# Kernel tuning notes

Measured on AMD Instinct MI355X. Metric: run time of the kernel, lower is better.

Reference implementation:

```python
import math
import jax, jax.numpy as jnp
import numpy as np

MODEL_DIM = 2048
NUM_HEADS = 16
HEAD_DIM = MODEL_DIM // NUM_HEADS
B, T = 4, 2048


def setup_inputs() -> dict:
    key = jax.random.key(0)
    ks = jax.random.split(key, 9)
    s = 0.02
    d = MODEL_DIM
    return {
        "x": jax.random.normal(ks[0], (B, T, d), dtype=jnp.float32),
        "wq": jax.random.normal(ks[1], (d, d), dtype=jnp.float32) * s,
        "bq": jnp.zeros((d,), dtype=jnp.float32),
        "wk": jax.random.normal(ks[2], (d, d), dtype=jnp.float32) * s,
        "bk": jnp.zeros((d,), dtype=jnp.float32),
        "wv": jax.random.normal(ks[3], (d, d), dtype=jnp.float32) * s,
        "bv": jnp.zeros((d,), dtype=jnp.float32),
        "wo": jax.random.normal(ks[4], (d, d), dtype=jnp.float32) * s,
        "bo": jnp.zeros((d,), dtype=jnp.float32),
    }


def reference(x, wq, bq, wk, bk, wv, bv, wo, bo):
    b, t, d = x.shape
    h, hd = NUM_HEADS, HEAD_DIM
    scale = 1.0 / math.sqrt(hd)
    # torch Linear: y = x @ W^T + b
    q = (x @ wq.T + bq).reshape(b, t, h, hd).transpose(0, 2, 1, 3)  # [B,H,T,hd]
    k = (x @ wk.T + bk).reshape(b, t, h, hd).transpose(0, 2, 1, 3)
    v = (x @ wv.T + bv).reshape(b, t, h, hd).transpose(0, 2, 1, 3)
    scores = jnp.einsum("bhqd,bhkd->bhqk", q, k) * scale  # [B,H,T,T]
    mask = jnp.tril(jnp.ones((t, t), dtype=bool))
    scores = jnp.where(mask[None, None], scores, -jnp.inf)
    probs = jax.nn.softmax(scores, axis=-1)
    out = jnp.einsum("bhqk,bhkd->bhqd", probs, v)  # [B,H,T,hd]
    out = out.transpose(0, 2, 1, 3).reshape(b, t, d)
    out = out @ wo.T + bo
    return (out, k, v)
```

## Files before the change

### kernel.cpp

```cpp
#include <hip/hip_runtime.h>
#include <hip/hip_bf16.h>
#include <stdint.h>

typedef __attribute__((ext_vector_type(8))) short short8;
typedef __attribute__((ext_vector_type(4))) float f32x4;

#define DEVI __device__ __forceinline__

DEVI unsigned short f2bf(float f) {
  union { float f; unsigned int u; } c; c.f = f;
  unsigned int u = c.u;
  u += 0x7fffu + ((u >> 16) & 1u);
  return (unsigned short)(u >> 16);
}

DEVI void gl_lds16(const void* gsrc, void* lds) {
  __builtin_amdgcn_global_load_lds(
      (const __attribute__((address_space(1))) unsigned int*)gsrc,
      (__attribute__((address_space(3))) unsigned int*)lds, 16, 0, 0);
}

#define MFMA(a, b, c) __builtin_amdgcn_mfma_f32_16x16x32_bf16((a), (b), (c), 0, 0, 0)

__global__ void cvt_f32_bf16(const float* __restrict__ in,
                             unsigned short* __restrict__ out, int n4) {
  const int stride = gridDim.x * blockDim.x;
  for (int i = blockIdx.x * blockDim.x + threadIdx.x; i < n4; i += stride) {
    const float4 v = ((const float4*)in)[i];
    ushort4 o;
    o.x = f2bf(v.x); o.y = f2bf(v.y); o.z = f2bf(v.z); o.w = f2bf(v.w);
    ((ushort4*)out)[i] = o;
  }
}


template<int MODE>
__global__ __launch_bounds__(512, 2)
void gemm256(const unsigned short* __restrict__ A,
             const unsigned short* __restrict__ Bw,
             const float* __restrict__ bq,
             const float* __restrict__ bk,
             const float* __restrict__ bv,
             float* __restrict__ Kf,
             float* __restrict__ Vf,
             unsigned short* __restrict__ Qpk,
             unsigned short* __restrict__ Kpk,
             unsigned short* __restrict__ Vpk,
             float* __restrict__ Cf,
             int M, int N, int K)
{
  __shared__ unsigned short S[4][16384];
  const int tid  = threadIdx.x;
  const int lane = tid & 63;
  const int wid  = tid >> 6;
  const int l15  = lane & 15, l4 = lane >> 4;

  const int chunk = gridDim.x >> 3;
  const int q  = blockIdx.x;
  const int wg = (q & 7) * chunk + (q >> 3);
  const int bm = (wg & 31) * 256;
  const int bn = (wg >> 5) * 256;

  const unsigned short* Asrc0 = A  + (size_t)(bm + wid * 16 + l15) * K + l4 * 8;
  const unsigned short* Asrc1 = A  + (size_t)(bm + (wid + 8) * 16 + l15) * K + l4 * 8;
  const unsigned short* Bsrc0 = Bw + (size_t)(bn + wid * 16 + l15) * K + l4 * 8;
  const unsigned short* Bsrc1 = Bw + (size_t)(bn + (wid + 8) * 16 + l15) * K + l4 * 8;

  const int nt = K >> 5;
#pragma unroll
  for (int kt = 0; kt < 3; ++kt) {
    unsigned short* Sd = S[kt];
    const int koff = kt * 32;
    gl_lds16(Asrc0 + koff, &Sd[wid * 512 + lane * 8]);
    gl_lds16(Asrc1 + koff, &Sd[(wid + 8) * 512 + lane * 8]);
    gl_lds16(Bsrc0 + koff, &Sd[8192 + wid * 512 + lane * 8]);
    gl_lds16(Bsrc1 + koff, &Sd[8192 + (wid + 8) * 512 + lane * 8]);
  }

  f32x4 acc[8][4] = {};
  const int afbase = (wid >> 2) * 4096 + lane * 8;
  const int bfbase = 8192 + (wid & 3) * 2048 + lane * 8;

  for (int kt = 0; kt < nt; ++kt) {
    const int rem = nt - 1 - kt;
    if (rem >= 2)      asm volatile("s_waitcnt vmcnt(8)" ::: "memory");
    else if (rem == 1) asm volatile("s_waitcnt vmcnt(4)" ::: "memory");
    else               asm volatile("s_waitcnt vmcnt(0)" ::: "memory");
    asm volatile("s_waitcnt lgkmcnt(0)" ::: "memory");
    __builtin_amdgcn_s_barrier();
    __builtin_amdgcn_sched_barrier(0);

    const unsigned short* Sb = S[kt & 3];
    short8 af[8], bf[4];
#pragma unroll
    for (int m = 0; m < 8; ++m) af[m] = *(const short8*)&Sb[afbase + m * 512];
#pragma unroll
    for (int n = 0; n < 4; ++n) bf[n] = *(const short8*)&Sb[bfbase + n * 512];

    if (kt + 3 < nt) {
      unsigned short* Sd = S[(kt + 3) & 3];
      const int koff = (kt + 3) * 32;
      gl_lds16(Asrc0 + koff, &Sd[wid * 512 + lane * 8]);
      gl_lds16(Asrc1 + koff, &Sd[(wid + 8) * 512 + lane * 8]);
      gl_lds16(Bsrc0 + koff, &Sd[8192 + wid * 512 + lane * 8]);
      gl_lds16(Bsrc1 + koff, &Sd[8192 + (wid + 8) * 512 + lane * 8]);
    }

    __builtin_amdgcn_s_setprio(1);
#pragma unroll
    for (int m = 0; m < 8; ++m)
#pragma unroll
      for (int n = 0; n < 4; ++n)
        acc[m][n] = MFMA(af[m], bf[n], acc[m][n]);
    __builtin_amdgcn_s_setprio(0);
  }

  const int rbase = l4 * 4;
#pragma unroll
  for (int m = 0; m < 8; ++m) {
    const int row0 = bm + (wid >> 2) * 128 + m * 16 + rbase;
#pragma unroll
    for (int n = 0; n < 4; ++n) {
      const int col6 = bn + (wid & 3) * 64 + n * 16 + l15;
      if constexpr (MODE == 3) {
        const float bb = bq[col6];
#pragma unroll
        for (int r = 0; r < 4; ++r)
          Cf[(size_t)(row0 + r) * N + col6] = acc[m][n][r] + bb;
      } else {
        const int sel = col6 >> 11;
        const int col = col6 & 2047;
        const float bb = (sel == 0 ? bq : sel == 1 ? bk : bv)[col];
        float vv[4];
#pragma unroll
        for (int r = 0; r < 4; ++r) vv[r] = acc[m][n][r] + bb;
        const int bI = row0 >> 11, t0 = row0 & 2047;
        const int h = col >> 7, e = col & 127;
        const size_t hb = ((size_t)(bI * 16 + h)) * 262144;
        if (sel == 0) {
          const size_t qb = hb + (size_t)(t0 >> 4) * 2048 + (e >> 5) * 512
                          + (t0 & 15) * 32 + (e & 31);
#pragma unroll
          for (int r = 0; r < 4; ++r) Qpk[qb + (size_t)r * 32] = f2bf(vv[r]);
        } else if (sel == 1) {
          const size_t idx = hb + (size_t)t0 * 128 + e;
          const size_t qb = hb + (size_t)(t0 >> 4) * 2048 + (e >> 5) * 512
                          + (t0 & 15) * 32 + (e & 31);
#pragma unroll
          for (int r = 0; r < 4; ++r) {
            Kf[idx + (size_t)r * 128] = vv[r];
            Kpk[qb + (size_t)r * 32] = f2bf(vv[r]);
          }
        } else {
          const size_t idx = hb + (size_t)t0 * 128 + e;
#pragma unroll
          for (int r = 0; r < 4; ++r) Vf[idx + (size_t)r * 128] = vv[r];
          const size_t vb = hb + (size_t)(t0 >> 6) * 8192 + (size_t)(e >> 4) * 1024
                          + ((t0 >> 5) & 1) * 512 + (e & 15) * 32 + (t0 & 31);
          ushort4 pk;
          pk.x = f2bf(vv[0]); pk.y = f2bf(vv[1]);
          pk.z = f2bf(vv[2]); pk.w = f2bf(vv[3]);
          *(ushort4*)&Vpk[vb] = pk;
        }
      }
    }
  }
}

__global__ __launch_bounds__(256, 2)
void attn_fwd(const unsigned short* __restrict__ Qf,
              const unsigned short* __restrict__ Kf,
              const unsigned short* __restrict__ Vf,
              unsigned short* __restrict__ Ab)
{
  constexpr float scale = 0.08838834764831843f;
  __shared__ unsigned short Pl[4][32][72];

  const int bid = blockIdx.x;
  const int idx = bid >> 3;
  const int bh  = (bid & 7) * 8 + (idx & 7);
  const int qb  = 15 - (idx >> 3);
  const int bI = bh >> 4, h = bh & 15;
  const int tid = threadIdx.x;
  const int wid = tid >> 6, lane = tid & 63;
  const int lr = lane & 15, lg = lane >> 4;
  const int lfo = lr * 32 + lg * 8;
  const int qw = qb * 128 + wid * 32;

  const unsigned short* Qp = Qf + (size_t)bh * 262144 + (size_t)(qw >> 4) * 2048;
  const unsigned short* Kp = Kf + (size_t)bh * 262144;
  const unsigned short* Vp = Vf + (size_t)bh * 262144;

  short8 qf[2][4];
#pragma unroll
  for (int m = 0; m < 2; ++m)
#pragma unroll
    for (int ks = 0; ks < 4; ++ks)
      qf[m][ks] = *(const short8*)&Qp[m * 2048 + ks * 512 + lfo];

  f32x4 o[2][8] = {};
  float mrun[2][4], lrun[2][4];
#pragma unroll
  for (int m = 0; m < 2; ++m)
#pragma unroll
    for (int r = 0; r < 4; ++r) { mrun[m][r] = -1e30f; lrun[m][r] = 0.f; }

  const int nfull = qw >> 6;
  for (int kt = 0; kt <= nfull; ++kt) {
    const int kv0 = kt * 64;
    const bool diag = (kt == nfull);
    const unsigned short* Kt = Kp + (size_t)(kv0 >> 4) * 2048;
    const unsigned short* Vt = Vp + (size_t)(kv0 >> 6) * 8192;

    short8 kf[4][4];
#pragma unroll
    for (int n = 0; n < 4; ++n)
#pragma unroll
      for (int ks = 0; ks < 4; ++ks)
        kf[n][ks] = *(const short8*)&Kt[n * 2048 + ks * 512 + lfo];
    f32x4 s[2][4] = {};
#pragma unroll
    for (int ks = 0; ks < 4; ++ks)
#pragma unroll
      for (int m = 0; m < 2; ++m)
#pragma unroll
        for (int n = 0; n < 4; ++n)
          s[m][n] = MFMA(qf[m][ks], kf[n][ks], s[m][n]);

    short8 vf[2][8];
#pragma unroll
    for (int ks2 = 0; ks2 < 2; ++ks2)
#pragma unroll
      for (int dt = 0; dt < 8; ++dt)
        vf[ks2][dt] = *(const short8*)&Vt[dt * 1024 + ks2 * 512 + lfo];

    float tmax[2][4];
#pragma unroll
    for (int m = 0; m < 2; ++m)
#pragma unroll
      for (int r = 0; r < 4; ++r) tmax[m][r] = -1e30f;
#pragma unroll
    for (int m = 0; m < 2; ++m)
#pragma unroll
      for (int n = 0; n < 4; ++n) {
        const int kg = kv0 + n * 16 + lr;
#pragma unroll
        for (int r = 0; r < 4; ++r) {
          float sv = s[m][n][r] * scale;
          if (diag) {
            const int qg = qw + m * 16 + lg * 4 + r;
            sv = (kg <= qg) ? sv : -1e30f;
          }
          s[m][n][r] = sv;
          tmax[m][r] = fmaxf(tmax[m][r], sv);
        }
      }
#pragma unroll
    for (int m = 0; m < 2; ++m)
#pragma unroll
      for (int r = 0; r < 4; ++r) {
#pragma unroll
        for (int off = 8; off >= 1; off >>= 1)
          tmax[m][r] = fmaxf(tmax[m][r], __shfl_xor(tmax[m][r], off));
        const float mnew  = fmaxf(mrun[m][r], tmax[m][r]);
        const float alpha = __expf(mrun[m][r] - mnew);
        mrun[m][r] = mnew;
        lrun[m][r] *= alpha;
#pragma unroll
        for (int d = 0; d < 8; ++d) o[m][d][r] *= alpha;
      }
#pragma unroll
    for (int m = 0; m < 2; ++m) {
      float ls[4] = {0.f, 0.f, 0.f, 0.f};
#pragma unroll
      for (int n = 0; n < 4; ++n)
#pragma unroll
        for (int r = 0; r < 4; ++r) {
          const float p = __expf(s[m][n][r] - mrun[m][r]);
          s[m][n][r] = p;
          ls[r] += p;
        }
#pragma unroll
      for (int r = 0; r < 4; ++r) {
#pragma unroll
        for (int off = 8; off >= 1; off >>= 1) ls[r] += __shfl_xor(ls[r], off);
        lrun[m][r] += ls[r];
      }
#pragma unroll
      for (int n = 0; n < 4; ++n)
#pragma unroll
        for (int r = 0; r < 4; ++r)
          Pl[wid][m * 16 + lg * 4 + r][n * 16 + lr] = f2bf(s[m][n][r]);
    }
#pragma unroll
    for (int ks2 = 0; ks2 < 2; ++ks2) {
      short8 pa[2];
#pragma unroll
      for (int m = 0; m < 2; ++m)
        pa[m] = *(const short8*)&Pl[wid][m * 16 + lr][ks2 * 32 + lg * 8];
#pragma unroll
      for (int dt = 0; dt < 8; ++dt)
#pragma unroll
        for (int m = 0; m < 2; ++m)
          o[m][dt] = MFMA(pa[m], vf[ks2][dt], o[m][dt]);
    }
  }
#pragma unroll
  for (int m = 0; m < 2; ++m)
#pragma unroll
    for (int r = 0; r < 4; ++r) {
      const float inv = 1.0f / lrun[m][r];
      const int t = qw + m * 16 + lg * 4 + r;
      unsigned short* dst = Ab + ((size_t)(bI * 2048 + t)) * 2048 + h * 128;
#pragma unroll
      for (int dt = 0; dt < 8; ++dt)
        dst[dt * 16 + lr] = f2bf(o[m][dt][r] * inv);
    }
}

extern "C" void kernel_launch(void* const* d_in, const int* in_sizes, int n_in,
                              void* d_out, int out_size, void* d_ws, size_t ws_size,
                              hipStream_t stream) {
  const float* x  = (const float*)d_in[0];
  const float* wq = (const float*)d_in[1];
  const float* bq = (const float*)d_in[2];
  const float* wk = (const float*)d_in[3];
  const float* bk = (const float*)d_in[4];
  const float* wv = (const float*)d_in[5];
  const float* bv = (const float*)d_in[6];
  const float* wo = (const float*)d_in[7];
  const float* bo = (const float*)d_in[8];

  float* out  = (float*)d_out;
  float* kout = out + (size_t)16777216;
  float* vout = out + (size_t)33554432;

  unsigned short* xb  = (unsigned short*)d_ws;
  unsigned short* wqb = xb  + 16777216;
  unsigned short* wkb = wqb + 4194304;
  unsigned short* wvb = wkb + 4194304;
  unsigned short* wob = wvb + 4194304;
  unsigned short* Qw  = wob + 4194304;
  unsigned short* Kw  = Qw  + 16777216;
  unsigned short* Vfw = Kw  + 16777216;
  unsigned short* Aw  = Vfw + 16777216;

  const int M = 8192, K = 2048;

  cvt_f32_bf16<<<1024, 256, 0, stream>>>(x,  xb,  4194304);
  cvt_f32_bf16<<<256,  256, 0, stream>>>(wq, wqb, 1048576);
  cvt_f32_bf16<<<256,  256, 0, stream>>>(wk, wkb, 1048576);
  cvt_f32_bf16<<<256,  256, 0, stream>>>(wv, wvb, 1048576);
  cvt_f32_bf16<<<256,  256, 0, stream>>>(wo, wob, 1048576);

  gemm256<0><<<dim3(768), 512, 0, stream>>>(xb, wqb, bq, bk, bv,
                                            kout, vout, Qw, Kw, Vfw,
                                            nullptr, M, 6144, K);

  attn_fwd<<<dim3(1024), 256, 0, stream>>>(Qw, Kw, Vfw, Aw);

  gemm256<3><<<dim3(256), 512, 0, stream>>>(Aw, wob, bo, nullptr, nullptr,
                                            nullptr, nullptr, nullptr, nullptr, nullptr,
                                            out, M, 2048, K);
}
```

Before: 575.1 us.

## Restructure GEMM into 8-phase ping-pong pipeline with 64-wide K tiles

```diff
diff --git a/kernel.cpp b/kernel.cpp
--- a/kernel.cpp
+++ b/kernel.cpp
@@ -21,6 +21,8 @@
 }
 
 #define MFMA(a, b, c) __builtin_amdgcn_mfma_f32_16x16x32_bf16((a), (b), (c), 0, 0, 0)
+#define BAR()  __builtin_amdgcn_s_barrier()
+#define SCHED0() __builtin_amdgcn_sched_barrier(0)
 
 __global__ void cvt_f32_bf16(const float* __restrict__ in,
                              unsigned short* __restrict__ out, int n4) {
@@ -36,24 +38,25 @@
 
 template<int MODE>
 __global__ __launch_bounds__(512, 2)
-void gemm256(const unsigned short* __restrict__ A,
-             const unsigned short* __restrict__ Bw,
-             const float* __restrict__ bq,
-             const float* __restrict__ bk,
-             const float* __restrict__ bv,
-             float* __restrict__ Kf,
-             float* __restrict__ Vf,
-             unsigned short* __restrict__ Qpk,
-             unsigned short* __restrict__ Kpk,
-             unsigned short* __restrict__ Vpk,
-             float* __restrict__ Cf,
-             int M, int N, int K)
+void gemm8p(const unsigned short* __restrict__ A,
+            const unsigned short* __restrict__ Bw,
+            const float* __restrict__ bq,
+            const float* __restrict__ bk,
+            const float* __restrict__ bv,
+            float* __restrict__ Kf,
+            float* __restrict__ Vf,
+            unsigned short* __restrict__ Qpk,
+            unsigned short* __restrict__ Kpk,
+            unsigned short* __restrict__ Vpk,
+            float* __restrict__ Cf,
+            int M, int N, int K)
 {
-  __shared__ unsigned short S[4][16384];
+  __shared__ unsigned short S[2][32768];
   const int tid  = threadIdx.x;
   const int lane = tid & 63;
   const int wid  = tid >> 6;
   const int l15  = lane & 15, l4 = lane >> 4;
+  const int wm   = wid >> 2, wn = wid & 3;
 
   const int chunk = gridDim.x >> 3;
   const int q  = blockIdx.x;
@@ -61,67 +64,123 @@
   const int bm = (wg & 31) * 256;
   const int bn = (wg >> 5) * 256;
 
-  const unsigned short* Asrc0 = A  + (size_t)(bm + wid * 16 + l15) * K + l4 * 8;
-  const unsigned short* Asrc1 = A  + (size_t)(bm + (wid + 8) * 16 + l15) * K + l4 * 8;
-  const unsigned short* Bsrc0 = Bw + (size_t)(bn + wid * 16 + l15) * K + l4 * 8;
-  const unsigned short* Bsrc1 = Bw + (size_t)(bn + (wid + 8) * 16 + l15) * K + l4 * 8;
-
-  const int nt = K >> 5;
-#pragma unroll
-  for (int kt = 0; kt < 3; ++kt) {
-    unsigned short* Sd = S[kt];
-    const int koff = kt * 32;
-    gl_lds16(Asrc0 + koff, &Sd[wid * 512 + lane * 8]);
-    gl_lds16(Asrc1 + koff, &Sd[(wid + 8) * 512 + lane * 8]);
-    gl_lds16(Bsrc0 + koff, &Sd[8192 + wid * 512 + lane * 8]);
-    gl_lds16(Bsrc1 + koff, &Sd[8192 + (wid + 8) * 512 + lane * 8]);
+  const unsigned short* Asrc = A  + (size_t)(bm + (wid >> 1) * 16 + l15) * K + (wid & 1) * 32 + l4 * 8;
+  const unsigned short* Bsrc = Bw + (size_t)(bn + (wid >> 1) * 16 + l15) * K + (wid & 1) * 32 + l4 * 8;
+
+  const int nKt   = K >> 6;
+  const int HTmax = nKt * 4;
+
+  auto stage_ht = [&](int g) {
+    if (g >= HTmax) return;
+    const int t = g >> 2, sub = g & 3, buf = t & 1, k0 = t << 6;
+#pragma unroll
+    for (int cc = 0; cc < 2; ++cc) {
+      if (sub >= 2) {
+        const int c = (sub - 2) * 2 + cc;
+        gl_lds16(Asrc + (size_t)(c * 64) * K + k0,
+                 &S[buf][c * 4096 + wid * 512 + lane * 8]);
+      } else {
+        const int c = sub * 2 + cc;
+        gl_lds16(Bsrc + (size_t)(c * 64) * K + k0,
+                 &S[buf][16384 + c * 4096 + wid * 512 + lane * 8]);
+      }
+    }
+  };
+
+#pragma unroll
+  for (int g = 0; g < 7; ++g) stage_ht(g);
+  asm volatile("s_waitcnt vmcnt(6)" ::: "memory");
+  SCHED0();
+  BAR();
+
+  f32x4 acc[8][4] = {};
+  short8 a[4][2], b[4][2];
+
+  for (int t = 0; t < nKt; ++t) {
+    const unsigned short* Sb = S[t & 1];
+    const int P = t * 4;
+
+#pragma unroll
+    for (int i = 0; i < 4; ++i)
+#pragma unroll
+      for (int ks = 0; ks < 2; ++ks)
+        a[i][ks] = *(const short8*)&Sb[((wm * 8 + i) * 2 + ks) * 512 + lane * 8];
+#pragma unroll
+    for (int j = 0; j < 4; ++j)
+#pragma unroll
+      for (int ks = 0; ks < 2; ++ks)
+        b[j][ks] = *(const short8*)&Sb[16384 + ((wn * 4 + j) * 2 + ks) * 512 + lane * 8];
+    stage_ht(P + 7);
+    BAR();
+    asm volatile("s_waitcnt lgkmcnt(0)" ::: "memory");
+    SCHED0();
+    __builtin_amdgcn_s_setprio(1);
+#pragma unroll
+    for (int i = 0; i < 4; ++i)
+#pragma unroll
+      for (int j = 0; j < 2; ++j)
+#pragma unroll
+        for (int ks = 0; ks < 2; ++ks)
+          acc[i][j] = MFMA(a[i][ks], b[j][ks], acc[i][j]);
+    __builtin_amdgcn_s_setprio(0);
+    BAR();
+
+    stage_ht(P + 8);
+    BAR();
+    __builtin_amdgcn_s_setprio(1);
+#pragma unroll
+    for (int i = 0; i < 4; ++i)
+#pragma unroll
+      for (int j = 0; j < 2; ++j)
+#pragma unroll
+        for (int ks = 0; ks < 2; ++ks)
+          acc[i][2 + j] = MFMA(a[i][ks], b[2 + j][ks], acc[i][2 + j]);
+    __builtin_amdgcn_s_setprio(0);
+    BAR();
+
+#pragma unroll
+    for (int i = 0; i < 4; ++i)
+#pragma unroll
+      for (int ks = 0; ks < 2; ++ks)
+        a[i][ks] = *(const short8*)&Sb[((wm * 8 + 4 + i) * 2 + ks) * 512 + lane * 8];
+    stage_ht(P + 9);
+    BAR();
+    asm volatile("s_waitcnt lgkmcnt(0)" ::: "memory");
+    SCHED0();
+    __builtin_amdgcn_s_setprio(1);
+#pragma unroll
+    for (int i = 0; i < 4; ++i)
+#pragma unroll
+      for (int j = 0; j < 2; ++j)
+#pragma unroll
+        for (int ks = 0; ks < 2; ++ks)
+          acc[4 + i][j] = MFMA(a[i][ks], b[j][ks], acc[4 + i][j]);
+    __builtin_amdgcn_s_setprio(0);
+    BAR();
+
+    stage_ht(P + 10);
+    if (t < nKt - 2)       { asm volatile("s_waitcnt vmcnt(6)" ::: "memory"); SCHED0(); }
+    else if (t == nKt - 2) { asm volatile("s_waitcnt vmcnt(0)" ::: "memory"); SCHED0(); }
+    BAR();
+    __builtin_amdgcn_s_setprio(1);
+#pragma unroll
+    for (int i = 0; i < 4; ++i)
+#pragma unroll
+      for (int j = 0; j < 2; ++j)
+#pragma unroll
+        for (int ks = 0; ks < 2; ++ks)
+          acc[4 + i][2 + j] = MFMA(a[i][ks], b[2 + j][ks], acc[4 + i][2 + j]);
+    __builtin_amdgcn_s_setprio(0);
+    BAR();
   }
 
-  f32x4 acc[8][4] = {};
-  const int afbase = (wid >> 2) * 4096 + lane * 8;
-  const int bfbase = 8192 + (wid & 3) * 2048 + lane * 8;
-
-  for (int kt = 0; kt < nt; ++kt) {
-    const int rem = nt - 1 - kt;
-    if (rem >= 2)      asm volatile("s_waitcnt vmcnt(8)" ::: "memory");
-    else if (rem == 1) asm volatile("s_waitcnt vmcnt(4)" ::: "memory");
-    else               asm volatile("s_waitcnt vmcnt(0)" ::: "memory");
-    asm volatile("s_waitcnt lgkmcnt(0)" ::: "memory");
-    __builtin_amdgcn_s_barrier();
-    __builtin_amdgcn_sched_barrier(0);
-
-    const unsigned short* Sb = S[kt & 3];
-    short8 af[8], bf[4];
-#pragma unroll
-    for (int m = 0; m < 8; ++m) af[m] = *(const short8*)&Sb[afbase + m * 512];
-#pragma unroll
-    for (int n = 0; n < 4; ++n) bf[n] = *(const short8*)&Sb[bfbase + n * 512];
-
-    if (kt + 3 < nt) {
-      unsigned short* Sd = S[(kt + 3) & 3];
-      const int koff = (kt + 3) * 32;
-      gl_lds16(Asrc0 + koff, &Sd[wid * 512 + lane * 8]);
-      gl_lds16(Asrc1 + koff, &Sd[(wid + 8) * 512 + lane * 8]);
-      gl_lds16(Bsrc0 + koff, &Sd[8192 + wid * 512 + lane * 8]);
-      gl_lds16(Bsrc1 + koff, &Sd[8192 + (wid + 8) * 512 + lane * 8]);
-    }
-
-    __builtin_amdgcn_s_setprio(1);
-#pragma unroll
-    for (int m = 0; m < 8; ++m)
-#pragma unroll
-      for (int n = 0; n < 4; ++n)
-        acc[m][n] = MFMA(af[m], bf[n], acc[m][n]);
-    __builtin_amdgcn_s_setprio(0);
-  }
-
   const int rbase = l4 * 4;
 #pragma unroll
   for (int m = 0; m < 8; ++m) {
-    const int row0 = bm + (wid >> 2) * 128 + m * 16 + rbase;
+    const int row0 = bm + wm * 128 + m * 16 + rbase;
 #pragma unroll
     for (int n = 0; n < 4; ++n) {
-      const int col6 = bn + (wid & 3) * 64 + n * 16 + l15;
+      const int col6 = bn + wn * 64 + n * 16 + l15;
       if constexpr (MODE == 3) {
         const float bb = bq[col6];
 #pragma unroll
@@ -353,13 +412,13 @@
   cvt_f32_bf16<<<256,  256, 0, stream>>>(wv, wvb, 1048576);
   cvt_f32_bf16<<<256,  256, 0, stream>>>(wo, wob, 1048576);
 
-  gemm256<0><<<dim3(768), 512, 0, stream>>>(xb, wqb, bq, bk, bv,
-                                            kout, vout, Qw, Kw, Vfw,
-                                            nullptr, M, 6144, K);
+  gemm8p<0><<<dim3(768), 512, 0, stream>>>(xb, wqb, bq, bk, bv,
+                                           kout, vout, Qw, Kw, Vfw,
+                                           nullptr, M, 6144, K);
 
   attn_fwd<<<dim3(1024), 256, 0, stream>>>(Qw, Kw, Vfw, Aw);
 
-  gemm256<3><<<dim3(256), 512, 0, stream>>>(Aw, wob, bo, nullptr, nullptr,
-                                            nullptr, nullptr, nullptr, nullptr, nullptr,
-                                            out, M, 2048, K);
-}
+  gemm8p<3><<<dim3(256), 512, 0, stream>>>(Aw, wob, bo, nullptr, nullptr,
+                                           nullptr, nullptr, nullptr, nullptr, nullptr,
+                                           out, M, 2048, K);
+}
```

Result: faster. 552.9 us (-3.9%).
